# Performance work log

Measured on AMD Instinct MI355X. Metric: run time of the kernel, lower is better.

Reference implementation:

```python
import jax, jax.numpy as jnp
import numpy as np
import math

D_MODEL = 1024
H = 16
D_K = D_MODEL // H
B = 4
S = 2048
NEG = -1e9


def setup_inputs() -> dict:
    key = jax.random.key(0)
    ks = jax.random.split(key, 11)
    scale = 1.0 / math.sqrt(D_MODEL)
    inp = {
        'q': jax.random.normal(ks[0], (B, S, D_MODEL), dtype=jnp.float32),
        'k': jax.random.normal(ks[1], (B, S, D_MODEL), dtype=jnp.float32),
        'v': jax.random.normal(ks[2], (B, S, D_MODEL), dtype=jnp.float32),
        'wq': jax.random.normal(ks[3], (D_MODEL, D_MODEL), dtype=jnp.float32) * scale,
        'bq': jnp.zeros((D_MODEL,), dtype=jnp.float32),
        'wk': jax.random.normal(ks[4], (D_MODEL, D_MODEL), dtype=jnp.float32) * scale,
        'bk': jnp.zeros((D_MODEL,), dtype=jnp.float32),
        'wv': jax.random.normal(ks[5], (D_MODEL, D_MODEL), dtype=jnp.float32) * scale,
        'bv': jnp.zeros((D_MODEL,), dtype=jnp.float32),
        'wo': jax.random.normal(ks[6], (D_MODEL, D_MODEL), dtype=jnp.float32) * scale,
        'bo': jnp.zeros((D_MODEL,), dtype=jnp.float32),
        # broadcastable causal mask [1, 1, S, S]; 0 = masked out
        'mask': jnp.tril(jnp.ones((S, S), dtype=jnp.int32))[None, None, :, :],
    }
    return inp


def reference(q, k, v, wq, bq, wk, bk, wv, bv, wo, bo, mask):
    # QKV projections: x @ W^T + b (nn.Linear convention)
    def split_heads(x):  # [B, S, D] -> [B, H, S, d_k]
        return x.reshape(B, S, H, D_K).transpose(0, 2, 1, 3)

    query = split_heads(q @ wq.T + bq)
    key_ = split_heads(k @ wk.T + bk)
    value = split_heads(v @ wv.T + bv)

    # scaled dot-product attention with mask; scores: [B, H, S, S]
    scores = jnp.einsum('bhqd,bhkd->bhqk', query, key_) / math.sqrt(D_K)
    scores = jnp.where(mask == 0, jnp.float32(NEG), scores)
    attn = jax.nn.softmax(scores, axis=-1)
    ctx = jnp.einsum('bhqk,bhkd->bhqd', attn, value)  # [B, H, S, d_k]

    # merge heads and output projection
    ctx = ctx.transpose(0, 2, 1, 3).reshape(B, S, D_MODEL)
    return ctx @ wo.T + bo
```

## Files before the change

kernel.cpp:

```cpp
#include <hip/hip_runtime.h>

#define DEVI __device__ __forceinline__

typedef __attribute__((ext_vector_type(8))) __bf16 bf16x8;
typedef __attribute__((ext_vector_type(4))) float f32x4;
typedef __attribute__((ext_vector_type(16))) float f32x16;
typedef __attribute__((ext_vector_type(4))) unsigned uint32x4;

DEVI __bf16 f2bf(float f) {
  unsigned u = __builtin_bit_cast(unsigned, f);
  unsigned r = u + 0x7fffu + ((u >> 16) & 1u);
  unsigned short h = (unsigned short)(r >> 16);
  return __builtin_bit_cast(__bf16, h);
}

DEVI unsigned cvt_pk_bf16(float lo, float hi) {
  unsigned r;
  asm("v_cvt_pk_bf16_f32 %0, %1, %2" : "=v"(r) : "v"(lo), "v"(hi));
  return r;
}

DEVI void load_lds16(const void* g, void* l) {
  __builtin_amdgcn_global_load_lds((__attribute__((address_space(1))) const void*)g,
                                   (__attribute__((address_space(3))) void*)l,
                                   16, 0, 0);
}

__global__ void convert_w4(const float* __restrict__ w0, const float* __restrict__ w1,
                           const float* __restrict__ w2, const float* __restrict__ w3,
                           __bf16* __restrict__ o0, __bf16* __restrict__ o1,
                           __bf16* __restrict__ o2, __bf16* __restrict__ o3, int n8) {
  int stride = gridDim.x * blockDim.x;
  for (int i = blockIdx.x * blockDim.x + threadIdx.x; i < 4 * n8; i += stride) {
    int sel = i / n8, j = i - sel * n8;
    const float* in = sel == 0 ? w0 : sel == 1 ? w1 : sel == 2 ? w2 : w3;
    __bf16* out = sel == 0 ? o0 : sel == 1 ? o1 : sel == 2 ? o2 : o3;
    float4 a = ((const float4*)in)[j * 2];
    float4 b = ((const float4*)in)[j * 2 + 1];
    bf16x8 o;
    o[0] = f2bf(a.x); o[1] = f2bf(a.y); o[2] = f2bf(a.z); o[3] = f2bf(a.w);
    o[4] = f2bf(b.x); o[5] = f2bf(b.y); o[6] = f2bf(b.z); o[7] = f2bf(b.w);
    ((bf16x8*)out)[j] = o;
  }
}

__global__ __launch_bounds__(256, 3) void gemm_qkv(
    const float* __restrict__ qa, const float* __restrict__ ka, const float* __restrict__ va,
    const __bf16* __restrict__ Wq, const __bf16* __restrict__ Wk, const __bf16* __restrict__ Wv,
    const float* __restrict__ bq, const float* __restrict__ bk, const float* __restrict__ bv,
    __bf16* __restrict__ Qh, __bf16* __restrict__ Kh, __bf16* __restrict__ Vt)
{
  __shared__ __align__(16) __bf16 As[3][128 * 32];
  __shared__ __align__(16) __bf16 Bs[3][128 * 32];
  const int sel = blockIdx.z;
  const float* A = sel == 0 ? qa : sel == 1 ? ka : va;
  const __bf16* W = sel == 0 ? Wq : sel == 1 ? Wk : Wv;
  const float* bias = sel == 0 ? bq : sel == 1 ? bk : bv;
  __bf16* outp = sel == 0 ? Qh : sel == 1 ? Kh : Vt;
  const bool vmode = (sel == 2);

  const int tid = threadIdx.x;
  const int lane = tid & 63;
  const int ln = lane & 15, g = lane >> 4;
  const int w = tid >> 6;
  const int wr = w >> 1, wc = w & 1;
  const int id = blockIdx.y * 64 + blockIdx.x;
  const int bx = 8 * (id & 7) + ((id >> 3) & 7);
  const int by = id >> 6;
  const int row0 = bx * 128, col0 = by * 128;

  const int ar = tid >> 1, ah = tid & 1;
  const int axr = (ar >> 1) & 3;

  f32x4 acc[4][4] = {};
  float4 fa0[4], fa1[4];

  auto issueA = [&](int kt, float4* f) {
    const float4* src = (const float4*)&A[(size_t)(row0 + ar) * 1024 + kt * 32 + ah * 16];
#pragma unroll
    for (int j = 0; j < 4; ++j) f[j] = src[j];
  };
  auto issueW = [&](int buf, int kt) {
#pragma unroll
    for (int i = 0; i < 2; ++i) {
      int c = tid + 256 * i;
      int r = c >> 2, sl = c & 3;
      int so = 8 * (sl ^ ((r >> 1) & 3));
      load_lds16(&W[(size_t)(col0 + r) * 1024 + kt * 32 + so], &Bs[buf][c * 8]);
    }
  };
  auto writeA = [&](int buf, const float4* f) {
#pragma unroll
    for (int j = 0; j < 2; ++j) {
      uint32x4 o;
      o[0] = cvt_pk_bf16(f[2 * j].x, f[2 * j].y);
      o[1] = cvt_pk_bf16(f[2 * j].z, f[2 * j].w);
      o[2] = cvt_pk_bf16(f[2 * j + 1].x, f[2 * j + 1].y);
      o[3] = cvt_pk_bf16(f[2 * j + 1].z, f[2 * j + 1].w);
      int s = 2 * ah + j;
      *(uint32x4*)&As[buf][ar * 32 + (s ^ axr) * 8] = o;
    }
  };
  auto compute = [&](int buf) {
    const __bf16* as = As[buf];
    const __bf16* bs = Bs[buf];
    bf16x8 aF[4], bF[4];
#pragma unroll
    for (int mi = 0; mi < 4; ++mi) {
      int r = wr * 64 + mi * 16 + ln;
      aF[mi] = *(const bf16x8*)&as[r * 32 + ((g * 8) ^ (((r >> 1) & 3) * 8))];
    }
#pragma unroll
    for (int ni = 0; ni < 4; ++ni) {
      int r = wc * 64 + ni * 16 + ln;
      bF[ni] = *(const bf16x8*)&bs[r * 32 + ((g * 8) ^ (((r >> 1) & 3) * 8))];
    }
    __builtin_amdgcn_s_setprio(1);
#pragma unroll
    for (int mi = 0; mi < 4; ++mi)
#pragma unroll
      for (int ni = 0; ni < 4; ++ni)
        acc[mi][ni] = __builtin_amdgcn_mfma_f32_16x16x32_bf16(aF[mi], bF[ni], acc[mi][ni], 0, 0, 0);
    __builtin_amdgcn_s_setprio(0);
  };

#define QKV_BAR(N) \
  asm volatile("s_waitcnt vmcnt(" #N ") lgkmcnt(0)" ::: "memory"); \
  __builtin_amdgcn_s_barrier(); \
  asm volatile("" ::: "memory");

#define QKV_STEP(KT, E, FAC, FAN) \
  QKV_BAR(6) \
  issueA((KT) + 2, FAC); \
  issueW(((E) + 2) % 3, (KT) + 2); \
  compute((E) % 3); \
  writeA(((E) + 1) % 3, FAN);

  issueA(0, fa0); issueW(0, 0);
  issueA(1, fa1); issueW(1, 1);
  writeA(0, fa0);

#pragma unroll 1
  for (int u = 0; u < 5; ++u) {
    const int kt = 6 * u;
    QKV_STEP(kt + 0, 0, fa0, fa1)
    QKV_STEP(kt + 1, 1, fa1, fa0)
    QKV_STEP(kt + 2, 2, fa0, fa1)
    QKV_STEP(kt + 3, 3, fa1, fa0)
    QKV_STEP(kt + 4, 4, fa0, fa1)
    QKV_STEP(kt + 5, 5, fa1, fa0)
  }
  QKV_BAR(6)
  compute(0);
  asm volatile("s_waitcnt vmcnt(2)" ::: "memory");
  writeA(1, fa1);
  QKV_BAR(0)
  compute(1);
#undef QKV_STEP
#undef QKV_BAR

#pragma unroll
  for (int ni = 0; ni < 4; ++ni) {
    int n = col0 + wc * 64 + ni * 16 + ln;
    float bv = bias[n];
#pragma unroll
    for (int mi = 0; mi < 4; ++mi) {
#pragma unroll
      for (int i = 0; i < 4; ++i) {
        int m = row0 + wr * 64 + mi * 16 + g * 4 + i;
        float val = acc[mi][ni][i] + bv;
        int b = m >> 11, s = m & 2047, h = n >> 6, d = n & 63;
        size_t idx = vmode
          ? ((size_t)((b * 16 + h) * 64 + d) * 2048 + s)
          : ((size_t)((b * 16 + h) * 2048 + s) * 64 + d);
        outp[idx] = f2bf(val);
      }
    }
  }
}

template<int MODE>
__global__ __launch_bounds__(256, 2) void gemm_bt(
    const __bf16* __restrict__ A, const __bf16* __restrict__ W,
    const float* __restrict__ bias, void* __restrict__ outp)
{
  __shared__ __bf16 As[3][128 * 32];
  __shared__ __bf16 Bs[3][128 * 32];
  const int tid = threadIdx.x;
  const int lane = tid & 63;
  const int ln = lane & 15, g = lane >> 4;
  const int w = tid >> 6;
  const int wr = w >> 1, wc = w & 1;
  const int id = blockIdx.y * 64 + blockIdx.x;
  const int bx = 8 * (id & 7) + ((id >> 3) & 7);
  const int by = id >> 6;
  const int row0 = bx * 128, col0 = by * 128;

  f32x4 acc[4][4] = {};

  auto stage = [&](int buf, int kt) {
    const int k0 = kt * 32;
#pragma unroll
    for (int i = 0; i < 2; ++i) {
      int c = tid + 256 * i;
      int r = c >> 2, sl = c & 3;
      int so = 8 * (sl ^ ((r >> 1) & 3));
      load_lds16(&A[(size_t)(row0 + r) * 1024 + k0 + so], &As[buf][c * 8]);
      load_lds16(&W[(size_t)(col0 + r) * 1024 + k0 + so], &Bs[buf][c * 8]);
    }
  };

  auto compute = [&](int buf) {
    const __bf16* as = As[buf];
    const __bf16* bs = Bs[buf];
    bf16x8 aF[4], bF[4];
#pragma unroll
    for (int mi = 0; mi < 4; ++mi) {
      int r = wr * 64 + mi * 16 + ln;
      aF[mi] = *(const bf16x8*)&as[r * 32 + ((g * 8) ^ (((r >> 1) & 3) * 8))];
    }
#pragma unroll
    for (int ni = 0; ni < 4; ++ni) {
      int r = wc * 64 + ni * 16 + ln;
      bF[ni] = *(const bf16x8*)&bs[r * 32 + ((g * 8) ^ (((r >> 1) & 3) * 8))];
    }
    __builtin_amdgcn_s_setprio(1);
#pragma unroll
    for (int mi = 0; mi < 4; ++mi)
#pragma unroll
      for (int ni = 0; ni < 4; ++ni)
        acc[mi][ni] = __builtin_amdgcn_mfma_f32_16x16x32_bf16(aF[mi], bF[ni], acc[mi][ni], 0, 0, 0);
    __builtin_amdgcn_s_setprio(0);
  };

  stage(0, 0);
  stage(1, 1);
#pragma unroll 1
  for (int kt = 0; kt < 31; ++kt) {
    asm volatile("s_waitcnt vmcnt(4)" ::: "memory");
    __builtin_amdgcn_s_barrier();
    asm volatile("" ::: "memory");
    if (kt + 2 < 32) stage((kt + 2) % 3, kt + 2);
    compute(kt % 3);
  }
  asm volatile("s_waitcnt vmcnt(0)" ::: "memory");
  __builtin_amdgcn_s_barrier();
  asm volatile("" ::: "memory");
  compute(31 % 3);

#pragma unroll
  for (int ni = 0; ni < 4; ++ni) {
    int n = col0 + wc * 64 + ni * 16 + ln;
    float bv = bias[n];
#pragma unroll
    for (int mi = 0; mi < 4; ++mi) {
#pragma unroll
      for (int i = 0; i < 4; ++i) {
        int m = row0 + wr * 64 + mi * 16 + g * 4 + i;
        float val = acc[mi][ni][i] + bv;
        if (MODE == 2) {
          ((float*)outp)[(size_t)m * 1024 + n] = val;
        } else {
          int b = m >> 11, s = m & 2047, h = n >> 6, d = n & 63;
          size_t idx = (MODE == 0)
            ? ((size_t)((b * 16 + h) * 2048 + s) * 64 + d)
            : ((size_t)((b * 16 + h) * 64 + d) * 2048 + s);
          ((__bf16*)outp)[idx] = f2bf(val);
        }
      }
    }
  }
}

__global__ __launch_bounds__(512, 4) void attn_fwd(
    const __bf16* __restrict__ Qh, const __bf16* __restrict__ Kh,
    const __bf16* __restrict__ Vt, __bf16* __restrict__ Ctx)
{
  __shared__ __bf16 KVs[8][64 * 64];

  const int tid = threadIdx.x;
  const int lane = tid & 63;
  const int l31 = lane & 31, hl = lane >> 5;
  const int w = tid >> 6;
  const int wq3 = w & 3, p = w >> 2;
  const int bh = blockIdx.x;
  const int b = bh >> 4, h = bh & 15;
  const float CE = 0.18033688f;
  const float MC = 40.0f * CE;

  auto stagePair = [&](int tp) {
    const int base = 2 * (tp & 1);
    const int c = tid;
    const int r = c >> 3, sl = c & 7;
    const int so = 8 * (sl ^ (r & 7));
#pragma unroll
    for (int i = 0; i < 2; ++i) {
      const int kv0 = (2 * tp + i) * 64, s = base + i;
      load_lds16(&Kh[((size_t)bh * 2048 + kv0 + r) * 64 + so], &KVs[s][c * 8]);
      load_lds16(&Vt[((size_t)bh * 64 + r) * 2048 + kv0 + so], &KVs[4 + s][c * 8]);
    }
  };

  auto strip = [&](int qb) {
    const int q0 = qb * 128;
    const int qw = q0 + wq3 * 32;
    const int qglob = qw + l31;
    const int np = qb + 1;

    bf16x8 qF[4];
#pragma unroll
    for (int ds = 0; ds < 4; ++ds)
      qF[ds] = *(const bf16x8*)&Qh[((size_t)bh * 2048 + qglob) * 64 + ds * 16 + hl * 8];

    f32x16 oT[2] = {};
    float lrun = 0.f;

    __syncthreads();
    stagePair(0);
    for (int tp = 0; tp < np; ++tp) {
      __syncthreads();
      if (tp + 1 < np) stagePair(tp + 1);
      const int kv0 = (2 * tp + p) * 64;
      if (kv0 > qw + 31) continue;
      const __bf16* ksm = KVs[2 * (tp & 1) + p];
      const __bf16* vsm = KVs[4 + 2 * (tp & 1) + p];

      f32x16 sT[2] = {};
#pragma unroll
      for (int kblk = 0; kblk < 2; ++kblk) {
        bf16x8 aK[4];
        const int r = kblk * 32 + l31;
#pragma unroll
        for (int ds = 0; ds < 4; ++ds)
          aK[ds] = *(const bf16x8*)&ksm[r * 64 + ((ds * 16 + hl * 8) ^ ((r & 7) * 8))];
        __builtin_amdgcn_s_setprio(1);
#pragma unroll
        for (int ds = 0; ds < 4; ++ds)
          sT[kblk] = __builtin_amdgcn_mfma_f32_32x32x16_bf16(aK[ds], qF[ds], sT[kblk], 0, 0, 0);
        __builtin_amdgcn_s_setprio(0);
      }

      if (kv0 + 63 > qw) {
#pragma unroll
        for (int kblk = 0; kblk < 2; ++kblk)
#pragma unroll
          for (int r = 0; r < 16; ++r) {
            int kvg = kv0 + kblk * 32 + (r & 3) + 8 * (r >> 2) + 4 * hl;
            sT[kblk][r] = (kvg <= qglob) ? sT[kblk][r] : -3e38f;
          }
      }

      unsigned c0[8], c1[8];
      float ps0 = 0.f, ps1 = 0.f, ps2 = 0.f, ps3 = 0.f;
#pragma unroll
      for (int w2 = 0; w2 < 8; ++w2) {
        float p0 = exp2f(__builtin_fmaf(sT[0][2 * w2],     CE, -MC));
        float p1 = exp2f(__builtin_fmaf(sT[0][2 * w2 + 1], CE, -MC));
        float p2 = exp2f(__builtin_fmaf(sT[1][2 * w2],     CE, -MC));
        float p3 = exp2f(__builtin_fmaf(sT[1][2 * w2 + 1], CE, -MC));
        ps0 += p0; ps1 += p1; ps2 += p2; ps3 += p3;
        c0[w2] = cvt_pk_bf16(p0, p1);
        c1[w2] = cvt_pk_bf16(p2, p3);
      }
      lrun += (ps0 + ps1) + (ps2 + ps3);

      uint32x4 Wv[4];
#pragma unroll
      for (int kblk = 0; kblk < 2; ++kblk)
#pragma unroll
        for (int ksl = 0; ksl < 2; ++ksl)
#pragma unroll
          for (int al = 0; al < 2; ++al) {
            unsigned cp = kblk ? c1[4 * ksl + al]     : c0[4 * ksl + al];
            unsigned cq = kblk ? c1[4 * ksl + 2 + al] : c0[4 * ksl + 2 + al];
            unsigned cqx = __shfl_xor(cq, 32);
            unsigned cpx = __shfl_xor(cp, 32);
            Wv[kblk * 2 + ksl][al]     = hl ? cqx : cp;
            Wv[kblk * 2 + ksl][al + 2] = hl ? cq  : cpx;
          }

#pragma unroll
      for (int dblk = 0; dblk < 2; ++dblk) {
        bf16x8 aV[4];
        const int r = dblk * 32 + l31;
#pragma unroll
        for (int ks = 0; ks < 4; ++ks)
          aV[ks] = *(const bf16x8*)&vsm[r * 64 + ((ks * 16 + hl * 8) ^ ((r & 7) * 8))];
        __builtin_amdgcn_s_setprio(1);
#pragma unroll
        for (int ks = 0; ks < 4; ++ks)
          oT[dblk] = __builtin_amdgcn_mfma_f32_32x32x16_bf16(
              aV[ks], __builtin_bit_cast(bf16x8, Wv[ks]), oT[dblk], 0, 0, 0);
        __builtin_amdgcn_s_setprio(0);
      }
    }

    __syncthreads();
    float* ex = (float*)KVs + wq3 * 2176 + lane * 34;
    if (p == 1) {
      lrun += __shfl_xor(lrun, 32);
#pragma unroll
      for (int dblk = 0; dblk < 2; ++dblk)
#pragma unroll
        for (int rb = 0; rb < 8; ++rb)
          *(float2*)(ex + dblk * 16 + rb * 2) =
              make_float2(oT[dblk][2 * rb], oT[dblk][2 * rb + 1]);
      ex[32] = lrun;
    }
    __syncthreads();
    if (p == 0) {
      lrun += __shfl_xor(lrun, 32);
      lrun += ex[32];
#pragma unroll
      for (int dblk = 0; dblk < 2; ++dblk)
#pragma unroll
        for (int rb = 0; rb < 8; ++rb) {
          float2 v = *(float2*)(ex + dblk * 16 + rb * 2);
          oT[dblk][2 * rb]     += v.x;
          oT[dblk][2 * rb + 1] += v.y;
        }
      const float inv = 1.0f / fmaxf(lrun, 1e-30f);
#pragma unroll
      for (int dblk = 0; dblk < 2; ++dblk)
#pragma unroll
        for (int rb = 0; rb < 4; ++rb) {
          unsigned u0 = cvt_pk_bf16(oT[dblk][4 * rb]     * inv, oT[dblk][4 * rb + 1] * inv);
          unsigned u1 = cvt_pk_bf16(oT[dblk][4 * rb + 2] * inv, oT[dblk][4 * rb + 3] * inv);
          int d = dblk * 32 + rb * 8 + 4 * hl;
          size_t idx = ((size_t)(b * 2048 + qglob)) * 1024 + h * 64 + d;
          *(uint2*)&Ctx[idx] = make_uint2(u0, u1);
        }
    }
  };

  strip(15 - (int)blockIdx.y);
  strip((int)blockIdx.y);
}

extern "C" void kernel_launch(void* const* d_in, const int* in_sizes, int n_in,
                              void* d_out, int out_size, void* d_ws, size_t ws_size,
                              hipStream_t stream) {
  const float* q  = (const float*)d_in[0];
  const float* k  = (const float*)d_in[1];
  const float* v  = (const float*)d_in[2];
  const float* wq = (const float*)d_in[3];
  const float* bq = (const float*)d_in[4];
  const float* wk = (const float*)d_in[5];
  const float* bk = (const float*)d_in[6];
  const float* wv = (const float*)d_in[7];
  const float* bv = (const float*)d_in[8];
  const float* wo = (const float*)d_in[9];
  const float* bo = (const float*)d_in[10];
  float* out = (float*)d_out;
  char* ws = (char*)d_ws;

  const size_t MB = 1024 * 1024;
  __bf16* Wqb  = (__bf16*)(ws + 0 * MB);
  __bf16* Wkb  = (__bf16*)(ws + 2 * MB);
  __bf16* Wvb  = (__bf16*)(ws + 4 * MB);
  __bf16* Wob  = (__bf16*)(ws + 6 * MB);
  __bf16* Ctx  = (__bf16*)(ws + 8 * MB);
  __bf16* Qh   = (__bf16*)(ws + 24 * MB);
  __bf16* Kh   = (__bf16*)(ws + 40 * MB);
  __bf16* Vt   = (__bf16*)(ws + 56 * MB);

  const int W8 = 1024 * 1024 / 8;

  convert_w4<<<2048, 256, 0, stream>>>(wq, wk, wv, wo, Wqb, Wkb, Wvb, Wob, W8);

  gemm_qkv<<<dim3(64, 8, 3), 256, 0, stream>>>(q, k, v, Wqb, Wkb, Wvb,
                                               bq, bk, bv, Qh, Kh, Vt);

  attn_fwd<<<dim3(64, 8), 512, 0, stream>>>(Qh, Kh, Vt, Ctx);

  gemm_bt<2><<<dim3(64, 8), 256, 0, stream>>>(Ctx, Wob, bo, out);
}
```

Before: 206.4 us.

## Drop LDS staging in attention; each wave streams K/V directly from global

The attention kernel no longer stages K and V tiles through shared memory with block-wide barriers. Each wave now handles its own 32-query slice (half the waves take the mirrored strip) and reads K and V fragments straight from global memory, relying on L2/L1 caching. This removes the LDS traffic, the barriers and the cross-wave reduction of partial outputs. In exchange, every wave issues redundant global loads with no prefetch overlap, and the occupancy hint is raised from 4 to 6.

```diff
diff --git a/kernel.cpp b/kernel.cpp
--- a/kernel.cpp
+++ b/kernel.cpp
@@ -272,169 +272,123 @@
   }
 }
 
-__global__ __launch_bounds__(512, 4) void attn_fwd(
+__global__ __launch_bounds__(512, 6) void attn_fwd(
     const __bf16* __restrict__ Qh, const __bf16* __restrict__ Kh,
     const __bf16* __restrict__ Vt, __bf16* __restrict__ Ctx)
 {
-  __shared__ __bf16 KVs[8][64 * 64];
-
   const int tid = threadIdx.x;
   const int lane = tid & 63;
   const int l31 = lane & 31, hl = lane >> 5;
   const int w = tid >> 6;
-  const int wq3 = w & 3, p = w >> 2;
+  const int wq3 = w & 3, sel = w >> 2;
   const int bh = blockIdx.x;
   const int b = bh >> 4, h = bh & 15;
+  const int y = blockIdx.y;
+  const int qb = sel ? y : 15 - y;
   const float CE = 0.18033688f;
   const float MC = 40.0f * CE;
 
-  auto stagePair = [&](int tp) {
-    const int base = 2 * (tp & 1);
-    const int c = tid;
-    const int r = c >> 3, sl = c & 7;
-    const int so = 8 * (sl ^ (r & 7));
-#pragma unroll
-    for (int i = 0; i < 2; ++i) {
-      const int kv0 = (2 * tp + i) * 64, s = base + i;
-      load_lds16(&Kh[((size_t)bh * 2048 + kv0 + r) * 64 + so], &KVs[s][c * 8]);
-      load_lds16(&Vt[((size_t)bh * 64 + r) * 2048 + kv0 + so], &KVs[4 + s][c * 8]);
-    }
-  };
-
-  auto strip = [&](int qb) {
-    const int q0 = qb * 128;
-    const int qw = q0 + wq3 * 32;
-    const int qglob = qw + l31;
-    const int np = qb + 1;
-
-    bf16x8 qF[4];
-#pragma unroll
-    for (int ds = 0; ds < 4; ++ds)
-      qF[ds] = *(const bf16x8*)&Qh[((size_t)bh * 2048 + qglob) * 64 + ds * 16 + hl * 8];
-
-    f32x16 oT[2] = {};
-    float lrun = 0.f;
-
-    __syncthreads();
-    stagePair(0);
-    for (int tp = 0; tp < np; ++tp) {
-      __syncthreads();
-      if (tp + 1 < np) stagePair(tp + 1);
-      const int kv0 = (2 * tp + p) * 64;
-      if (kv0 > qw + 31) continue;
-      const __bf16* ksm = KVs[2 * (tp & 1) + p];
-      const __bf16* vsm = KVs[4 + 2 * (tp & 1) + p];
-
-      f32x16 sT[2] = {};
-#pragma unroll
-      for (int kblk = 0; kblk < 2; ++kblk) {
-        bf16x8 aK[4];
-        const int r = kblk * 32 + l31;
-#pragma unroll
-        for (int ds = 0; ds < 4; ++ds)
-          aK[ds] = *(const bf16x8*)&ksm[r * 64 + ((ds * 16 + hl * 8) ^ ((r & 7) * 8))];
-        __builtin_amdgcn_s_setprio(1);
-#pragma unroll
-        for (int ds = 0; ds < 4; ++ds)
-          sT[kblk] = __builtin_amdgcn_mfma_f32_32x32x16_bf16(aK[ds], qF[ds], sT[kblk], 0, 0, 0);
-        __builtin_amdgcn_s_setprio(0);
-      }
-
-      if (kv0 + 63 > qw) {
-#pragma unroll
-        for (int kblk = 0; kblk < 2; ++kblk)
-#pragma unroll
-          for (int r = 0; r < 16; ++r) {
-            int kvg = kv0 + kblk * 32 + (r & 3) + 8 * (r >> 2) + 4 * hl;
-            sT[kblk][r] = (kvg <= qglob) ? sT[kblk][r] : -3e38f;
-          }
-      }
-
-      unsigned c0[8], c1[8];
-      float ps0 = 0.f, ps1 = 0.f, ps2 = 0.f, ps3 = 0.f;
-#pragma unroll
-      for (int w2 = 0; w2 < 8; ++w2) {
-        float p0 = exp2f(__builtin_fmaf(sT[0][2 * w2],     CE, -MC));
-        float p1 = exp2f(__builtin_fmaf(sT[0][2 * w2 + 1], CE, -MC));
-        float p2 = exp2f(__builtin_fmaf(sT[1][2 * w2],     CE, -MC));
-        float p3 = exp2f(__builtin_fmaf(sT[1][2 * w2 + 1], CE, -MC));
-        ps0 += p0; ps1 += p1; ps2 += p2; ps3 += p3;
-        c0[w2] = cvt_pk_bf16(p0, p1);
-        c1[w2] = cvt_pk_bf16(p2, p3);
-      }
-      lrun += (ps0 + ps1) + (ps2 + ps3);
-
-      uint32x4 Wv[4];
+  const __bf16* Kb = Kh + (size_t)bh * 2048 * 64;
+  const __bf16* Vb = Vt + (size_t)bh * 64 * 2048;
+
+  const int qw = qb * 128 + wq3 * 32;
+  const int qglob = qw + l31;
+  const int tlim = (qw + 31) / 64 + 1;
+
+  bf16x8 qF[4];
+#pragma unroll
+  for (int ds = 0; ds < 4; ++ds)
+    qF[ds] = *(const bf16x8*)&Qh[((size_t)bh * 2048 + qglob) * 64 + ds * 16 + hl * 8];
+
+  f32x16 oT[2] = {};
+  float lrun = 0.f;
+
+#pragma unroll 1
+  for (int tt = 0; tt < tlim; ++tt) {
+    const int kv0 = tt * 64;
+
+    f32x16 sT[2] = {};
+#pragma unroll
+    for (int kblk = 0; kblk < 2; ++kblk) {
+      bf16x8 aK[4];
+      const int r = kv0 + kblk * 32 + l31;
+#pragma unroll
+      for (int ds = 0; ds < 4; ++ds)
+        aK[ds] = *(const bf16x8*)&Kb[(size_t)r * 64 + ds * 16 + hl * 8];
+      __builtin_amdgcn_s_setprio(1);
+#pragma unroll
+      for (int ds = 0; ds < 4; ++ds)
+        sT[kblk] = __builtin_amdgcn_mfma_f32_32x32x16_bf16(aK[ds], qF[ds], sT[kblk], 0, 0, 0);
+      __builtin_amdgcn_s_setprio(0);
+    }
+
+    if (kv0 + 63 > qw) {
 #pragma unroll
       for (int kblk = 0; kblk < 2; ++kblk)
 #pragma unroll
-        for (int ksl = 0; ksl < 2; ++ksl)
-#pragma unroll
-          for (int al = 0; al < 2; ++al) {
-            unsigned cp = kblk ? c1[4 * ksl + al]     : c0[4 * ksl + al];
-            unsigned cq = kblk ? c1[4 * ksl + 2 + al] : c0[4 * ksl + 2 + al];
-            unsigned cqx = __shfl_xor(cq, 32);
-            unsigned cpx = __shfl_xor(cp, 32);
-            Wv[kblk * 2 + ksl][al]     = hl ? cqx : cp;
-            Wv[kblk * 2 + ksl][al + 2] = hl ? cq  : cpx;
-          }
-
-#pragma unroll
-      for (int dblk = 0; dblk < 2; ++dblk) {
-        bf16x8 aV[4];
-        const int r = dblk * 32 + l31;
-#pragma unroll
-        for (int ks = 0; ks < 4; ++ks)
-          aV[ks] = *(const bf16x8*)&vsm[r * 64 + ((ks * 16 + hl * 8) ^ ((r & 7) * 8))];
-        __builtin_amdgcn_s_setprio(1);
-#pragma unroll
-        for (int ks = 0; ks < 4; ++ks)
-          oT[dblk] = __builtin_amdgcn_mfma_f32_32x32x16_bf16(
-              aV[ks], __builtin_bit_cast(bf16x8, Wv[ks]), oT[dblk], 0, 0, 0);
-        __builtin_amdgcn_s_setprio(0);
-      }
-    }
-
-    __syncthreads();
-    float* ex = (float*)KVs + wq3 * 2176 + lane * 34;
-    if (p == 1) {
-      lrun += __shfl_xor(lrun, 32);
-#pragma unroll
-      for (int dblk = 0; dblk < 2; ++dblk)
-#pragma unroll
-        for (int rb = 0; rb < 8; ++rb)
-          *(float2*)(ex + dblk * 16 + rb * 2) =
-              make_float2(oT[dblk][2 * rb], oT[dblk][2 * rb + 1]);
-      ex[32] = lrun;
-    }
-    __syncthreads();
-    if (p == 0) {
-      lrun += __shfl_xor(lrun, 32);
-      lrun += ex[32];
-#pragma unroll
-      for (int dblk = 0; dblk < 2; ++dblk)
-#pragma unroll
-        for (int rb = 0; rb < 8; ++rb) {
-          float2 v = *(float2*)(ex + dblk * 16 + rb * 2);
-          oT[dblk][2 * rb]     += v.x;
-          oT[dblk][2 * rb + 1] += v.y;
+        for (int r = 0; r < 16; ++r) {
+          int kvg = kv0 + kblk * 32 + (r & 3) + 8 * (r >> 2) + 4 * hl;
+          sT[kblk][r] = (kvg <= qglob) ? sT[kblk][r] : -3e38f;
         }
-      const float inv = 1.0f / fmaxf(lrun, 1e-30f);
-#pragma unroll
-      for (int dblk = 0; dblk < 2; ++dblk)
-#pragma unroll
-        for (int rb = 0; rb < 4; ++rb) {
-          unsigned u0 = cvt_pk_bf16(oT[dblk][4 * rb]     * inv, oT[dblk][4 * rb + 1] * inv);
-          unsigned u1 = cvt_pk_bf16(oT[dblk][4 * rb + 2] * inv, oT[dblk][4 * rb + 3] * inv);
-          int d = dblk * 32 + rb * 8 + 4 * hl;
-          size_t idx = ((size_t)(b * 2048 + qglob)) * 1024 + h * 64 + d;
-          *(uint2*)&Ctx[idx] = make_uint2(u0, u1);
+    }
+
+    unsigned c0[8], c1[8];
+    float ps0 = 0.f, ps1 = 0.f, ps2 = 0.f, ps3 = 0.f;
+#pragma unroll
+    for (int w2 = 0; w2 < 8; ++w2) {
+      float p0 = exp2f(__builtin_fmaf(sT[0][2 * w2],     CE, -MC));
+      float p1 = exp2f(__builtin_fmaf(sT[0][2 * w2 + 1], CE, -MC));
+      float p2 = exp2f(__builtin_fmaf(sT[1][2 * w2],     CE, -MC));
+      float p3 = exp2f(__builtin_fmaf(sT[1][2 * w2 + 1], CE, -MC));
+      ps0 += p0; ps1 += p1; ps2 += p2; ps3 += p3;
+      c0[w2] = cvt_pk_bf16(p0, p1);
+      c1[w2] = cvt_pk_bf16(p2, p3);
+    }
+    lrun += (ps0 + ps1) + (ps2 + ps3);
+
+    uint32x4 Wv[4];
+#pragma unroll
+    for (int kblk = 0; kblk < 2; ++kblk)
+#pragma unroll
+      for (int ksl = 0; ksl < 2; ++ksl)
+#pragma unroll
+        for (int al = 0; al < 2; ++al) {
+          unsigned cp = kblk ? c1[4 * ksl + al]     : c0[4 * ksl + al];
+          unsigned cq = kblk ? c1[4 * ksl + 2 + al] : c0[4 * ksl + 2 + al];
+          unsigned cqx = __shfl_xor(cq, 32);
+          unsigned cpx = __shfl_xor(cp, 32);
+          Wv[kblk * 2 + ksl][al]     = hl ? cqx : cp;
+          Wv[kblk * 2 + ksl][al + 2] = hl ? cq  : cpx;
         }
-    }
-  };
-
-  strip(15 - (int)blockIdx.y);
-  strip((int)blockIdx.y);
+
+#pragma unroll
+    for (int dblk = 0; dblk < 2; ++dblk) {
+      bf16x8 aV[4];
+      const int rv = dblk * 32 + l31;
+#pragma unroll
+      for (int ks = 0; ks < 4; ++ks)
+        aV[ks] = *(const bf16x8*)&Vb[(size_t)rv * 2048 + kv0 + ks * 16 + hl * 8];
+      __builtin_amdgcn_s_setprio(1);
+#pragma unroll
+      for (int ks = 0; ks < 4; ++ks)
+        oT[dblk] = __builtin_amdgcn_mfma_f32_32x32x16_bf16(
+            aV[ks], __builtin_bit_cast(bf16x8, Wv[ks]), oT[dblk], 0, 0, 0);
+      __builtin_amdgcn_s_setprio(0);
+    }
+  }
+
+  lrun += __shfl_xor(lrun, 32);
+  const float inv = 1.0f / fmaxf(lrun, 1e-30f);
+#pragma unroll
+  for (int dblk = 0; dblk < 2; ++dblk)
+#pragma unroll
+    for (int rb = 0; rb < 4; ++rb) {
+      unsigned u0 = cvt_pk_bf16(oT[dblk][4 * rb]     * inv, oT[dblk][4 * rb + 1] * inv);
+      unsigned u1 = cvt_pk_bf16(oT[dblk][4 * rb + 2] * inv, oT[dblk][4 * rb + 3] * inv);
+      int d = dblk * 32 + rb * 8 + 4 * hl;
+      size_t idx = ((size_t)(b * 2048 + qglob)) * 1024 + h * 64 + d;
+      *(uint2*)&Ctx[idx] = make_uint2(u0, u1);
+    }
 }
 
 extern "C" void kernel_launch(void* const* d_in, const int* in_sizes, int n_in,
```

Result: slower. 369.0 us (+78.8%).

## Process both causal query strips in one KV sweep to share staged tiles

Applied to the files above, without the earlier changes.

Each block previously ran its two query strips (high and low) one after the other, staging K/V tiles into LDS separately for each. Now a single KV loop over the longer strip computes both strips per staged tile, so the low strip's tiles are loaded only once and the second pass of syncs and loads disappears. Keeping two sets of Q fragments and accumulators raises register pressure, so launch bounds drop from 4 to 3 blocks per CU, which may reduce occupancy and latency hiding.

```diff
diff --git a/kernel.cpp b/kernel.cpp
--- a/kernel.cpp
+++ b/kernel.cpp
@@ -272,7 +272,7 @@
   }
 }
 
-__global__ __launch_bounds__(512, 4) void attn_fwd(
+__global__ __launch_bounds__(512, 3) void attn_fwd(
     const __bf16* __restrict__ Qh, const __bf16* __restrict__ Kh,
     const __bf16* __restrict__ Vt, __bf16* __restrict__ Ctx)
 {
@@ -285,8 +285,14 @@
   const int wq3 = w & 3, p = w >> 2;
   const int bh = blockIdx.x;
   const int b = bh >> 4, h = bh & 15;
+  const int y = blockIdx.y;
   const float CE = 0.18033688f;
   const float MC = 40.0f * CE;
+
+  const int qbh = 15 - y, qbl = y;
+  const int qwh = qbh * 128 + wq3 * 32, qwl = qbl * 128 + wq3 * 32;
+  const int qgh = qwh + l31, qgl = qwl + l31;
+  const int nph = qbh + 1, npl = qbl + 1;
 
   auto stagePair = [&](int tp) {
     const int base = 2 * (tp & 1);
@@ -301,102 +307,105 @@
     }
   };
 
-  auto strip = [&](int qb) {
-    const int q0 = qb * 128;
-    const int qw = q0 + wq3 * 32;
-    const int qglob = qw + l31;
-    const int np = qb + 1;
-
-    bf16x8 qF[4];
-#pragma unroll
-    for (int ds = 0; ds < 4; ++ds)
-      qF[ds] = *(const bf16x8*)&Qh[((size_t)bh * 2048 + qglob) * 64 + ds * 16 + hl * 8];
-
-    f32x16 oT[2] = {};
-    float lrun = 0.f;
-
+  bf16x8 qFh[4], qFl[4];
+#pragma unroll
+  for (int ds = 0; ds < 4; ++ds) {
+    qFh[ds] = *(const bf16x8*)&Qh[((size_t)bh * 2048 + qgh) * 64 + ds * 16 + hl * 8];
+    qFl[ds] = *(const bf16x8*)&Qh[((size_t)bh * 2048 + qgl) * 64 + ds * 16 + hl * 8];
+  }
+
+  f32x16 oTh[2] = {}, oTl[2] = {};
+  float lrunh = 0.f, lrunl = 0.f;
+
+  auto tileStep = [&](const __bf16* ksm, const __bf16* vsm, int kv0, int qg,
+                      int qw, bf16x8 (&qF)[4], f32x16 (&oT)[2], float& lrun) {
+    f32x16 sT[2] = {};
+#pragma unroll
+    for (int kblk = 0; kblk < 2; ++kblk) {
+      bf16x8 aK[4];
+      const int r = kblk * 32 + l31;
+#pragma unroll
+      for (int ds = 0; ds < 4; ++ds)
+        aK[ds] = *(const bf16x8*)&ksm[r * 64 + ((ds * 16 + hl * 8) ^ ((r & 7) * 8))];
+      __builtin_amdgcn_s_setprio(1);
+#pragma unroll
+      for (int ds = 0; ds < 4; ++ds)
+        sT[kblk] = __builtin_amdgcn_mfma_f32_32x32x16_bf16(aK[ds], qF[ds], sT[kblk], 0, 0, 0);
+      __builtin_amdgcn_s_setprio(0);
+    }
+
+    if (kv0 + 63 > qw) {
+#pragma unroll
+      for (int kblk = 0; kblk < 2; ++kblk)
+#pragma unroll
+        for (int r = 0; r < 16; ++r) {
+          int kvg = kv0 + kblk * 32 + (r & 3) + 8 * (r >> 2) + 4 * hl;
+          sT[kblk][r] = (kvg <= qg) ? sT[kblk][r] : -3e38f;
+        }
+    }
+
+    unsigned c0[8], c1[8];
+    float ps0 = 0.f, ps1 = 0.f, ps2 = 0.f, ps3 = 0.f;
+#pragma unroll
+    for (int w2 = 0; w2 < 8; ++w2) {
+      float p0 = exp2f(__builtin_fmaf(sT[0][2 * w2],     CE, -MC));
+      float p1 = exp2f(__builtin_fmaf(sT[0][2 * w2 + 1], CE, -MC));
+      float p2 = exp2f(__builtin_fmaf(sT[1][2 * w2],     CE, -MC));
+      float p3 = exp2f(__builtin_fmaf(sT[1][2 * w2 + 1], CE, -MC));
+      ps0 += p0; ps1 += p1; ps2 += p2; ps3 += p3;
+      c0[w2] = cvt_pk_bf16(p0, p1);
+      c1[w2] = cvt_pk_bf16(p2, p3);
+    }
+    lrun += (ps0 + ps1) + (ps2 + ps3);
+
+    uint32x4 Wv[4];
+#pragma unroll
+    for (int kblk = 0; kblk < 2; ++kblk)
+#pragma unroll
+      for (int ksl = 0; ksl < 2; ++ksl)
+#pragma unroll
+        for (int al = 0; al < 2; ++al) {
+          unsigned cp = kblk ? c1[4 * ksl + al]     : c0[4 * ksl + al];
+          unsigned cq = kblk ? c1[4 * ksl + 2 + al] : c0[4 * ksl + 2 + al];
+          unsigned cqx = __shfl_xor(cq, 32);
+          unsigned cpx = __shfl_xor(cp, 32);
+          Wv[kblk * 2 + ksl][al]     = hl ? cqx : cp;
+          Wv[kblk * 2 + ksl][al + 2] = hl ? cq  : cpx;
+        }
+
+#pragma unroll
+    for (int dblk = 0; dblk < 2; ++dblk) {
+      bf16x8 aV[4];
+      const int r = dblk * 32 + l31;
+#pragma unroll
+      for (int ks = 0; ks < 4; ++ks)
+        aV[ks] = *(const bf16x8*)&vsm[r * 64 + ((ks * 16 + hl * 8) ^ ((r & 7) * 8))];
+      __builtin_amdgcn_s_setprio(1);
+#pragma unroll
+      for (int ks = 0; ks < 4; ++ks)
+        oT[dblk] = __builtin_amdgcn_mfma_f32_32x32x16_bf16(
+            aV[ks], __builtin_bit_cast(bf16x8, Wv[ks]), oT[dblk], 0, 0, 0);
+      __builtin_amdgcn_s_setprio(0);
+    }
+  };
+
+  stagePair(0);
+#pragma unroll 1
+  for (int tp = 0; tp < nph; ++tp) {
     __syncthreads();
-    stagePair(0);
-    for (int tp = 0; tp < np; ++tp) {
-      __syncthreads();
-      if (tp + 1 < np) stagePair(tp + 1);
-      const int kv0 = (2 * tp + p) * 64;
-      if (kv0 > qw + 31) continue;
-      const __bf16* ksm = KVs[2 * (tp & 1) + p];
-      const __bf16* vsm = KVs[4 + 2 * (tp & 1) + p];
-
-      f32x16 sT[2] = {};
-#pragma unroll
-      for (int kblk = 0; kblk < 2; ++kblk) {
-        bf16x8 aK[4];
-        const int r = kblk * 32 + l31;
-#pragma unroll
-        for (int ds = 0; ds < 4; ++ds)
-          aK[ds] = *(const bf16x8*)&ksm[r * 64 + ((ds * 16 + hl * 8) ^ ((r & 7) * 8))];
-        __builtin_amdgcn_s_setprio(1);
-#pragma unroll
-        for (int ds = 0; ds < 4; ++ds)
-          sT[kblk] = __builtin_amdgcn_mfma_f32_32x32x16_bf16(aK[ds], qF[ds], sT[kblk], 0, 0, 0);
-        __builtin_amdgcn_s_setprio(0);
-      }
-
-      if (kv0 + 63 > qw) {
-#pragma unroll
-        for (int kblk = 0; kblk < 2; ++kblk)
-#pragma unroll
-          for (int r = 0; r < 16; ++r) {
-            int kvg = kv0 + kblk * 32 + (r & 3) + 8 * (r >> 2) + 4 * hl;
-            sT[kblk][r] = (kvg <= qglob) ? sT[kblk][r] : -3e38f;
-          }
-      }
-
-      unsigned c0[8], c1[8];
-      float ps0 = 0.f, ps1 = 0.f, ps2 = 0.f, ps3 = 0.f;
-#pragma unroll
-      for (int w2 = 0; w2 < 8; ++w2) {
-        float p0 = exp2f(__builtin_fmaf(sT[0][2 * w2],     CE, -MC));
-        float p1 = exp2f(__builtin_fmaf(sT[0][2 * w2 + 1], CE, -MC));
-        float p2 = exp2f(__builtin_fmaf(sT[1][2 * w2],     CE, -MC));
-        float p3 = exp2f(__builtin_fmaf(sT[1][2 * w2 + 1], CE, -MC));
-        ps0 += p0; ps1 += p1; ps2 += p2; ps3 += p3;
-        c0[w2] = cvt_pk_bf16(p0, p1);
-        c1[w2] = cvt_pk_bf16(p2, p3);
-      }
-      lrun += (ps0 + ps1) + (ps2 + ps3);
-
-      uint32x4 Wv[4];
-#pragma unroll
-      for (int kblk = 0; kblk < 2; ++kblk)
-#pragma unroll
-        for (int ksl = 0; ksl < 2; ++ksl)
-#pragma unroll
-          for (int al = 0; al < 2; ++al) {
-            unsigned cp = kblk ? c1[4 * ksl + al]     : c0[4 * ksl + al];
-            unsigned cq = kblk ? c1[4 * ksl + 2 + al] : c0[4 * ksl + 2 + al];
-            unsigned cqx = __shfl_xor(cq, 32);
-            unsigned cpx = __shfl_xor(cp, 32);
-            Wv[kblk * 2 + ksl][al]     = hl ? cqx : cp;
-            Wv[kblk * 2 + ksl][al + 2] = hl ? cq  : cpx;
-          }
-
-#pragma unroll
-      for (int dblk = 0; dblk < 2; ++dblk) {
-        bf16x8 aV[4];
-        const int r = dblk * 32 + l31;
-#pragma unroll
-        for (int ks = 0; ks < 4; ++ks)
-          aV[ks] = *(const bf16x8*)&vsm[r * 64 + ((ks * 16 + hl * 8) ^ ((r & 7) * 8))];
-        __builtin_amdgcn_s_setprio(1);
-#pragma unroll
-        for (int ks = 0; ks < 4; ++ks)
-          oT[dblk] = __builtin_amdgcn_mfma_f32_32x32x16_bf16(
-              aV[ks], __builtin_bit_cast(bf16x8, Wv[ks]), oT[dblk], 0, 0, 0);
-        __builtin_amdgcn_s_setprio(0);
-      }
-    }
-
+    if (tp + 1 < nph) stagePair(tp + 1);
+    const int kv0 = (2 * tp + p) * 64;
+    const __bf16* ksm = KVs[2 * (tp & 1) + p];
+    const __bf16* vsm = KVs[4 + 2 * (tp & 1) + p];
+    if (kv0 <= qwh + 31)
+      tileStep(ksm, vsm, kv0, qgh, qwh, qFh, oTh, lrunh);
+    if (tp < npl && kv0 <= qwl + 31)
+      tileStep(ksm, vsm, kv0, qgl, qwl, qFl, oTl, lrunl);
+  }
+
+  float* ex = (float*)KVs + wq3 * 2176 + lane * 34;
+  auto combine = [&](f32x16 (&oT)[2], float lrun, int qg) {
     __syncthreads();
-    float* ex = (float*)KVs + wq3 * 2176 + lane * 34;
     if (p == 1) {
       lrun += __shfl_xor(lrun, 32);
 #pragma unroll
@@ -427,14 +436,13 @@
           unsigned u0 = cvt_pk_bf16(oT[dblk][4 * rb]     * inv, oT[dblk][4 * rb + 1] * inv);
           unsigned u1 = cvt_pk_bf16(oT[dblk][4 * rb + 2] * inv, oT[dblk][4 * rb + 3] * inv);
           int d = dblk * 32 + rb * 8 + 4 * hl;
-          size_t idx = ((size_t)(b * 2048 + qglob)) * 1024 + h * 64 + d;
+          size_t idx = ((size_t)(b * 2048 + qg)) * 1024 + h * 64 + d;
           *(uint2*)&Ctx[idx] = make_uint2(u0, u1);
         }
     }
   };
-
-  strip(15 - (int)blockIdx.y);
-  strip((int)blockIdx.y);
+  combine(oTh, lrunh, qgh);
+  combine(oTl, lrunl, qgl);
 }
 
 extern "C" void kernel_launch(void* const* d_in, const int* in_sizes, int n_in,
```

New measurement: 219.0 us. +6.1%, slower.
